# Kernel tuning notes

Measured on AMD Instinct MI355X. Metric: run time of the kernel, lower is better.

Reference implementation:

```python
import jax, jax.numpy as jnp
import numpy as np

R = 0.5  # init kwarg r; reduction='mean'
N = 8192


def setup_inputs() -> dict:
    key = jax.random.key(0)
    k1, k2, k3 = jax.random.split(key, 3)
    pred = jax.random.normal(k1, (N, 1), dtype=jnp.float32)
    time = jax.random.uniform(k2, (N,), dtype=jnp.float32) * 100.0  # survival times
    event = jax.random.randint(k3, (N,), 0, 2).astype(jnp.float32)  # censoring indicator in {0,1}
    target = jnp.stack([time, event], axis=1)  # [N, 2]
    return {"pred": pred, "target": target}


def reference(pred, target):
    p = pred.squeeze(-1)            # [n]
    time = target[:, 0]             # [n]
    event = target[:, 1]            # [n]

    diff = p - time
    diff = jnp.where(event == 0, jnp.maximum(diff, 0.0), diff)
    regression_loss = jnp.mean(diff * diff)

    # ranking branch over all n^2 ordered pairs (i=index2 slow, j=index1 fast):
    # valid pair iff time[j] > time[i] and event[i] == 1
    mask = (time[None, :] > time[:, None]) & (event[:, None] == 1)  # [n, n] bool
    hinge = jnp.maximum(1.0 - p[None, :] + p[:, None], 0.0)         # [n, n]
    cnt = jnp.maximum(mask.sum(), 1).astype(jnp.float32)            # dynamic pair count -> masked mean
    ranking_loss = jnp.sum(jnp.where(mask, hinge * hinge, 0.0)) / cnt

    return R * ranking_loss + (1.0 - R) * regression_loss
```

## Files before the change

kernel.cpp:

```cpp
#include <hip/hip_runtime.h>

#define BLK 256
#define KJ 4
#define JLANES (BLK * KJ)
#define ITILE 64
#define IB 16
#define GX (8192 / ITILE)
#define GY (8192 / JLANES)
#define NSLOTS (GX * GY)

__global__ __launch_bounds__(BLK) void svm_partial(
    const float* __restrict__ pred,
    const float2* __restrict__ tg,
    float4* __restrict__ ws_slots) {
  const int tid = threadIdx.x;
  const int i0 = blockIdx.x * ITILE;
  const int j0 = blockIdx.y * JLANES;

  float pj[KJ], tj[KJ];
  #pragma unroll
  for (int k = 0; k < KJ; ++k) {
    pj[k] = pred[j0 + tid + k * BLK];
    tj[k] = tg[j0 + tid + k * BLK].x;
  }

  float rank = 0.0f;
  unsigned int cnt = 0u;

  for (int ib = 0; ib < ITILE; ib += IB) {
    float pi[IB], ti[IB], ei[IB];
    #pragma unroll
    for (int u = 0; u < IB; ++u) {
      pi[u] = pred[i0 + ib + u];
      float2 te = tg[i0 + ib + u];
      ti[u] = te.x;
      ei[u] = te.y;
    }
    #pragma unroll
    for (int u = 0; u < IB; ++u) {
      if (ei[u] == 1.0f) {
        const float pi1 = pi[u] + 1.0f;
        #pragma unroll
        for (int k = 0; k < KJ; ++k) {
          const bool m = tj[k] > ti[u];
          cnt += (unsigned int)__popcll(__ballot(m));
          float h = fmaxf(pi1 - pj[k], 0.0f);
          h = m ? h : 0.0f;
          rank = fmaf(h, h, rank);
        }
      }
    }
  }

  float reg = 0.0f;
  if (blockIdx.y == 0 && tid < ITILE) {
    const int i = i0 + tid;
    const float p = pred[i];
    const float2 te = tg[i];
    float d = p - te.x;
    if (te.y == 0.0f) d = fmaxf(d, 0.0f);
    reg = d * d;
  }

  #pragma unroll
  for (int off = 32; off > 0; off >>= 1) {
    rank += __shfl_down(rank, off);
    reg  += __shfl_down(reg, off);
  }

  __shared__ float sr[BLK / 64];
  __shared__ float sg[BLK / 64];
  __shared__ unsigned int sc[BLK / 64];
  const int wave = tid >> 6;
  const int lane = tid & 63;
  if (lane == 0) { sr[wave] = rank; sg[wave] = reg; sc[wave] = cnt; }
  __syncthreads();

  if (tid == 0) {
    const float r = sr[0] + sr[1] + sr[2] + sr[3];
    const float g = sg[0] + sg[1] + sg[2] + sg[3];
    const unsigned int c = sc[0] + sc[1] + sc[2] + sc[3];
    const int slot = blockIdx.y * GX + blockIdx.x;
    ws_slots[slot] = make_float4(r, g, (float)c, 0.0f);
  }
}

__global__ __launch_bounds__(64) void svm_finalize(
    const float4* __restrict__ ws_slots,
    float* __restrict__ out, int n) {
  const int tid = threadIdx.x;
  double r = 0.0, g = 0.0, c = 0.0;
  #pragma unroll
  for (int s = tid; s < NSLOTS; s += 64) {
    const float4 v = ws_slots[s];
    r += (double)v.x;
    g += (double)v.y;
    c += (double)v.z;
  }
  #pragma unroll
  for (int off = 32; off > 0; off >>= 1) {
    r += __shfl_down(r, off);
    g += __shfl_down(g, off);
    c += __shfl_down(c, off);
  }
  if (tid == 0) {
    const double cd = (c > 0.0 ? c : 1.0);
    out[0] = (float)(0.5 * r / cd + 0.5 * g / (double)n);
  }
}

extern "C" void kernel_launch(void* const* d_in, const int* in_sizes, int n_in,
                              void* d_out, int out_size, void* d_ws, size_t ws_size,
                              hipStream_t stream) {
  const float* pred = (const float*)d_in[0];
  const float2* tg = (const float2*)d_in[1];
  float* out = (float*)d_out;
  const int n = in_sizes[0];

  float4* ws_slots = (float4*)d_ws;

  svm_partial<<<dim3(GX, GY), BLK, 0, stream>>>(pred, tg, ws_slots);
  svm_finalize<<<1, 64, 0, stream>>>(ws_slots, out, n);
}
```

Before: 67.37 us.

## Retile pairwise loop with more j per thread, vectorized loads, split accumulators

Raises the number of j elements held per thread from 4 to 16 and shrinks the i-tile from 64 to 16, so the grid becomes 512x2 blocks instead of 128x8. The j values are now loaded with contiguous float4 vector loads per thread rather than strided scalar loads. The rank sum is split into two independent accumulators to shorten the FMA dependency chain. The aim is more arithmetic per loaded i value and better memory efficiency, at the cost of higher register pressure and more blocks each doing a small amount of i work.

After: 72.64 us. +7.8%, slower.

```diff
diff --git a/kernel.cpp b/kernel.cpp
--- a/kernel.cpp
+++ b/kernel.cpp
@@ -1,10 +1,9 @@
 #include <hip/hip_runtime.h>
 
 #define BLK 256
-#define KJ 4
+#define KJ 16
 #define JLANES (BLK * KJ)
-#define ITILE 64
-#define IB 16
+#define ITILE 16
 #define GX (8192 / ITILE)
 #define GY (8192 / JLANES)
 #define NSLOTS (GX * GY)
@@ -18,39 +17,59 @@
   const int j0 = blockIdx.y * JLANES;
 
   float pj[KJ], tj[KJ];
-  #pragma unroll
-  for (int k = 0; k < KJ; ++k) {
-    pj[k] = pred[j0 + tid + k * BLK];
-    tj[k] = tg[j0 + tid + k * BLK].x;
+  {
+    const float4* p4 = reinterpret_cast<const float4*>(pred + j0 + tid * KJ);
+    #pragma unroll
+    for (int q = 0; q < KJ / 4; ++q) {
+      const float4 v = p4[q];
+      pj[4 * q + 0] = v.x; pj[4 * q + 1] = v.y;
+      pj[4 * q + 2] = v.z; pj[4 * q + 3] = v.w;
+    }
+    const float4* t4 = reinterpret_cast<const float4*>(
+        reinterpret_cast<const float*>(tg) + 2 * (j0 + tid * KJ));
+    #pragma unroll
+    for (int q = 0; q < KJ / 2; ++q) {
+      const float4 v = t4[q];
+      tj[2 * q + 0] = v.x; tj[2 * q + 1] = v.z;
+    }
   }
 
-  float rank = 0.0f;
+  float pi[ITILE], ti[ITILE], ei[ITILE];
+  #pragma unroll
+  for (int u = 0; u < ITILE; ++u) {
+    pi[u] = pred[i0 + u];
+    const float2 te = tg[i0 + u];
+    ti[u] = te.x; ei[u] = te.y;
+  }
+
+  float rank0 = 0.0f, rank1 = 0.0f;
   unsigned int cnt = 0u;
 
-  for (int ib = 0; ib < ITILE; ib += IB) {
-    float pi[IB], ti[IB], ei[IB];
-    #pragma unroll
-    for (int u = 0; u < IB; ++u) {
-      pi[u] = pred[i0 + ib + u];
-      float2 te = tg[i0 + ib + u];
-      ti[u] = te.x;
-      ei[u] = te.y;
-    }
-    #pragma unroll
-    for (int u = 0; u < IB; ++u) {
-      if (ei[u] == 1.0f) {
-        const float pi1 = pi[u] + 1.0f;
-        #pragma unroll
-        for (int k = 0; k < KJ; ++k) {
-          const bool m = tj[k] > ti[u];
+  #pragma unroll
+  for (int u = 0; u < ITILE; ++u) {
+    if (ei[u] == 1.0f) {
+      const float pi1 = pi[u] + 1.0f;
+      const float tu = ti[u];
+      #pragma unroll
+      for (int k = 0; k < KJ; k += 2) {
+        {
+          const bool m = tj[k] > tu;
           cnt += (unsigned int)__popcll(__ballot(m));
           float h = fmaxf(pi1 - pj[k], 0.0f);
           h = m ? h : 0.0f;
-          rank = fmaf(h, h, rank);
+          rank0 = fmaf(h, h, rank0);
+        }
+        {
+          const bool m = tj[k + 1] > tu;
+          cnt += (unsigned int)__popcll(__ballot(m));
+          float h = fmaxf(pi1 - pj[k + 1], 0.0f);
+          h = m ? h : 0.0f;
+          rank1 = fmaf(h, h, rank1);
         }
       }
     }
   }
+  float rank = rank0 + rank1;
 
   float reg = 0.0f;
   if (blockIdx.y == 0 && tid < ITILE) {
```

## Fuse finalize into partial kernel via last-block spin on flagged slots

Applied to the files above, without the earlier changes.

Removes the separate finalize launch. Each block publishes its partials plus a magic flag using release atomics, and the last-indexed block spins until every flag is set, then reduces and resets the flags. This saves a kernel launch and its gap. The cost is a spin-wait that assumes all blocks eventually run concurrently or finish before the last block is scheduled, which risks deadlock or waiting if block scheduling order differs.

New measurement: 74.10 us. +10.0%, slower.

```diff
diff --git a/kernel.cpp b/kernel.cpp
--- a/kernel.cpp
+++ b/kernel.cpp
@@ -8,11 +8,13 @@
 #define GX (8192 / ITILE)
 #define GY (8192 / JLANES)
 #define NSLOTS (GX * GY)
+#define MAGIC 0x1F2E3D4Cu
 
-__global__ __launch_bounds__(BLK) void svm_partial(
+__global__ __launch_bounds__(BLK) void svm_fused(
     const float* __restrict__ pred,
     const float2* __restrict__ tg,
-    float4* __restrict__ ws_slots) {
+    unsigned int* __restrict__ ws,
+    float* __restrict__ out, int n) {
   const int tid = threadIdx.x;
   const int i0 = blockIdx.x * ITILE;
   const int j0 = blockIdx.y * JLANES;
@@ -76,36 +78,56 @@
   if (lane == 0) { sr[wave] = rank; sg[wave] = reg; sc[wave] = cnt; }
   __syncthreads();
 
+  const int slot = blockIdx.y * GX + blockIdx.x;
+
   if (tid == 0) {
     const float r = sr[0] + sr[1] + sr[2] + sr[3];
     const float g = sg[0] + sg[1] + sg[2] + sg[3];
     const unsigned int c = sc[0] + sc[1] + sc[2] + sc[3];
-    const int slot = blockIdx.y * GX + blockIdx.x;
-    ws_slots[slot] = make_float4(r, g, (float)c, 0.0f);
+    unsigned int* s = ws + 4 * slot;
+    __hip_atomic_store(s + 0, __float_as_uint(r), __ATOMIC_RELAXED, __HIP_MEMORY_SCOPE_AGENT);
+    __hip_atomic_store(s + 1, __float_as_uint(g), __ATOMIC_RELAXED, __HIP_MEMORY_SCOPE_AGENT);
+    __hip_atomic_store(s + 2, c,                  __ATOMIC_RELAXED, __HIP_MEMORY_SCOPE_AGENT);
+    __hip_atomic_store(s + 3, MAGIC,              __ATOMIC_RELEASE, __HIP_MEMORY_SCOPE_AGENT);
   }
-}
 
-__global__ __launch_bounds__(64) void svm_finalize(
-    const float4* __restrict__ ws_slots,
-    float* __restrict__ out, int n) {
-  const int tid = threadIdx.x;
-  double r = 0.0, g = 0.0, c = 0.0;
-  #pragma unroll
-  for (int s = tid; s < NSLOTS; s += 64) {
-    const float4 v = ws_slots[s];
-    r += (double)v.x;
-    g += (double)v.y;
-    c += (double)v.z;
-  }
-  #pragma unroll
-  for (int off = 32; off > 0; off >>= 1) {
-    r += __shfl_down(r, off);
-    g += __shfl_down(g, off);
-    c += __shfl_down(c, off);
-  }
-  if (tid == 0) {
-    const double cd = (c > 0.0 ? c : 1.0);
-    out[0] = (float)(0.5 * r / cd + 0.5 * g / (double)n);
+  if (slot == NSLOTS - 1 && tid < 64) {
+    bool ready = false;
+    while (!ready) {
+      bool mine = true;
+      #pragma unroll
+      for (int q = 0; q < NSLOTS / 64; ++q) {
+        const int s = tid + q * 64;
+        const unsigned int f = __hip_atomic_load(ws + 4 * s + 3,
+                                                 __ATOMIC_ACQUIRE,
+                                                 __HIP_MEMORY_SCOPE_AGENT);
+        mine &= (f == MAGIC);
+      }
+      ready = (bool)__all(mine);
+    }
+
+    double r = 0.0, g = 0.0, c = 0.0;
+    #pragma unroll
+    for (int q = 0; q < NSLOTS / 64; ++q) {
+      const int s = tid + q * 64;
+      const unsigned int ur = __hip_atomic_load(ws + 4 * s + 0, __ATOMIC_RELAXED, __HIP_MEMORY_SCOPE_AGENT);
+      const unsigned int ug = __hip_atomic_load(ws + 4 * s + 1, __ATOMIC_RELAXED, __HIP_MEMORY_SCOPE_AGENT);
+      const unsigned int uc = __hip_atomic_load(ws + 4 * s + 2, __ATOMIC_RELAXED, __HIP_MEMORY_SCOPE_AGENT);
+      r += (double)__uint_as_float(ur);
+      g += (double)__uint_as_float(ug);
+      c += (double)uc;
+      __hip_atomic_store(ws + 4 * s + 3, 0u, __ATOMIC_RELAXED, __HIP_MEMORY_SCOPE_AGENT);
+    }
+    #pragma unroll
+    for (int off = 32; off > 0; off >>= 1) {
+      r += __shfl_down(r, off);
+      g += __shfl_down(g, off);
+      c += __shfl_down(c, off);
+    }
+    if (tid == 0) {
+      const double cd = (c > 0.0 ? c : 1.0);
+      out[0] = (float)(0.5 * r / cd + 0.5 * g / (double)n);
+    }
   }
 }
 
@@ -117,8 +139,7 @@
   float* out = (float*)d_out;
   const int n = in_sizes[0];
 
-  float4* ws_slots = (float4*)d_ws;
+  unsigned int* ws = (unsigned int*)d_ws;
 
-  svm_partial<<<dim3(GX, GY), BLK, 0, stream>>>(pred, tg, ws_slots);
-  svm_finalize<<<1, 64, 0, stream>>>(ws_slots, out, n);
+  svm_fused<<<dim3(GX, GY), BLK, 0, stream>>>(pred, tg, ws, out, n);
 }
```
